# Optimization experiments

Hardware: AMD Instinct MI355X
Metric: run time of the kernel (lower is better)

Reference implementation:

```python
import jax, jax.numpy as jnp
import numpy as np

HIDDEN = 512
DETER = 1024
STOCH = 32
OBS = 1024
ACT = 64
B, T = 64, 256


def _linear_params(key, out_dim, in_dim):
    kw, kb = jax.random.split(key)
    scale = 1.0 / np.sqrt(in_dim)
    W = jax.random.uniform(kw, (out_dim, in_dim), jnp.float32, -scale, scale)
    b = jax.random.uniform(kb, (out_dim,), jnp.float32, -scale, scale)
    return W, b


def setup_inputs() -> dict:
    key = jax.random.key(0)
    ks = jax.random.split(key, 12)
    obs_embeds = jax.random.normal(ks[0], (B, T, OBS), jnp.float32)
    action_embs = jax.random.normal(ks[1], (B, T, ACT), jnp.float32)
    noise_prior = jax.random.normal(ks[2], (B, T, STOCH), jnp.float32)
    noise_post = jax.random.normal(ks[3], (B, T, STOCH), jnp.float32)
    W_sa, b_sa = _linear_params(ks[4], DETER, STOCH + ACT)
    W_ih, b_ih = _linear_params(ks[5], 3 * DETER, DETER)
    W_hh, b_hh = _linear_params(ks[6], 3 * DETER, DETER)
    Wp1, bp1 = _linear_params(ks[7], HIDDEN, DETER)
    Wp2, bp2 = _linear_params(ks[8], 2 * STOCH, HIDDEN)
    Wq1, bq1 = _linear_params(ks[9], HIDDEN, DETER + OBS)
    Wq2, bq2 = _linear_params(ks[10], 2 * STOCH, HIDDEN)
    return {
        "obs_embeds": obs_embeds, "action_embs": action_embs,
        "noise_prior": noise_prior, "noise_post": noise_post,
        "W_sa": W_sa, "b_sa": b_sa,
        "W_ih": W_ih, "b_ih": b_ih, "W_hh": W_hh, "b_hh": b_hh,
        "Wp1": Wp1, "bp1": bp1, "Wp2": Wp2, "bp2": bp2,
        "Wq1": Wq1, "bq1": bq1, "Wq2": Wq2, "bq2": bq2,
    }


def _rollout(obs_embeds, action_embs, noise_prior, noise_post,
             W_sa, b_sa, W_ih, b_ih, W_hh, b_hh,
             Wp1, bp1, Wp2, bp2, Wq1, bq1, Wq2, bq2):
    S = Wp2.shape[0] // 2
    eps = 1e-5

    def gru(x, h):  # torch GRUCell: gates ordered r, z, n
        gi = x @ W_ih.T + b_ih
        gh = h @ W_hh.T + b_hh
        ir, iz, inn = jnp.split(gi, 3, axis=-1)
        hr, hz, hn = jnp.split(gh, 3, axis=-1)
        r = jax.nn.sigmoid(ir + hr)
        z = jax.nn.sigmoid(iz + hz)
        n = jnp.tanh(inn + r * hn)
        return (1.0 - z) * n + z * h

    def step(carry, inp):
        deter, stoch = carry
        obs, act, n_p, n_q = inp
        # prior: h_t = f(s_{t-1}, a_{t-1}, h_{t-1})
        emb = jax.nn.relu(jnp.concatenate([stoch, act], -1) @ W_sa.T + b_sa)
        deter = gru(emb, deter)
        pm_s = jax.nn.relu(deter @ Wp1.T + bp1) @ Wp2.T + bp2
        p_mean = pm_s[..., :S]
        p_std = jax.nn.softplus(pm_s[..., S:]) + eps
        p_stoch = p_mean + p_std * n_p
        # posterior: p(s_t | h_t, o_t)
        qm_s = jax.nn.relu(jnp.concatenate([deter, obs], -1) @ Wq1.T + bq1) @ Wq2.T + bq2
        q_mean = qm_s[..., :S]
        q_std = jax.nn.softplus(qm_s[..., S:]) + eps
        q_stoch = q_mean + q_std * n_q
        out = jnp.concatenate([deter, p_mean, p_std, p_stoch, q_mean, q_std, q_stoch], -1)
        return (deter, q_stoch), out

    batch = obs_embeds.shape[0]
    deter0 = jnp.zeros((batch, W_hh.shape[1]), obs_embeds.dtype)
    stoch0 = jnp.zeros((batch, S), obs_embeds.dtype)
    xs = (
        jnp.swapaxes(obs_embeds, 0, 1),
        jnp.swapaxes(action_embs, 0, 1),
        jnp.swapaxes(noise_prior, 0, 1),
        jnp.swapaxes(noise_post, 0, 1),
    )
    _, outs = jax.lax.scan(step, (deter0, stoch0), xs)
    return jnp.swapaxes(outs, 0, 1)  # [B, T, deter + 6*stoch]


def reference(obs_embeds, action_embs, noise_prior, noise_post,
              W_sa, b_sa, W_ih, b_ih, W_hh, b_hh,
              Wp1, bp1, Wp2, bp2, Wq1, bq1, Wq2, bq2):
    return _rollout(obs_embeds, action_embs, noise_prior, noise_post,
                    W_sa, b_sa, W_ih, b_ih, W_hh, b_hh,
                    Wp1, bp1, Wp2, bp2, Wq1, bq1, Wq2, bq2)
```

## Files before the change

### kernel.cpp

```cpp
#include <hip/hip_runtime.h>
#include <math.h>

#define B_   64
#define T_   256
#define OUTD 1216
#define NBLK 64

typedef unsigned short ushort_t;
typedef unsigned int   uint32;
typedef unsigned long long u64;
typedef __attribute__((ext_vector_type(8))) short bfrag;
typedef __attribute__((ext_vector_type(4))) float f32x4;
typedef __attribute__((ext_vector_type(4))) unsigned short us4;

#define SCOPE_AGT __HIP_MEMORY_SCOPE_AGENT

__device__ __forceinline__ float sigmoidf_(float x) { return 1.0f / (1.0f + __expf(-x)); }
__device__ __forceinline__ float softplusf_(float x) { return (x > 20.0f) ? x : log1pf(__expf(x)); }
__device__ __forceinline__ ushort_t f2bf(float f) {
    uint32 u = __float_as_uint(f);
    u += 0x7fffu + ((u >> 16) & 1u);
    return (ushort_t)(u >> 16);
}
__device__ __forceinline__ float bf2f(ushort_t u) { return __uint_as_float(((uint32)u) << 16); }

union U16 { u64 q[2]; bfrag bv; f32x4 fv; };
union U8  { u64 q; us4 v4; };

__device__ __forceinline__ u64 ldc8(const void* p) {
    return __hip_atomic_load((const u64*)p, __ATOMIC_RELAXED, SCOPE_AGT);
}
__device__ __forceinline__ void stc8(void* p, u64 v) {
    __hip_atomic_store((u64*)p, v, __ATOMIC_RELAXED, SCOPE_AGT);
}
__device__ __forceinline__ f32x4 ldc16f(const void* p) {
    U16 u; u.q[0] = ldc8(p); u.q[1] = ldc8((const u64*)p + 1); return u.fv;
}
__device__ __forceinline__ void stc16f(void* p, f32x4 v) {
    U16 u; u.fv = v; stc8(p, u.q[0]); stc8((u64*)p + 1, u.q[1]);
}
__device__ __forceinline__ void stc16b(void* p, bfrag v) {
    U16 u; u.bv = v; stc8(p, u.q[0]); stc8((u64*)p + 1, u.q[1]);
}

__global__ void kwprep(const float* __restrict__ Wih, const float* __restrict__ Whh,
                       const float* __restrict__ Wp1, const float* __restrict__ Wq1,
                       const float* __restrict__ Wp2, const float* __restrict__ Wq2,
                       const float* __restrict__ Wsa,
                       ushort_t* Wih_b, ushort_t* Whh_b, ushort_t* Wp1_b, ushort_t* Wq1_b,
                       ushort_t* W2sw, ushort_t* Wsasw, unsigned* gsync) {
    int stride = gridDim.x * blockDim.x;
    int gid = blockIdx.x * blockDim.x + threadIdx.x;
    for (int i = gid; i < 4096; i += stride) gsync[i] = 0u;
    for (int i = gid; i < 3072 * 1024; i += stride) Wih_b[i] = f2bf(Wih[i]);
    for (int i = gid; i < 3072 * 1024; i += stride) Whh_b[i] = f2bf(Whh[i]);
    for (int i = gid; i < 512 * 1024; i += stride) Wp1_b[i] = f2bf(Wp1[i]);
    for (int i = gid; i < 512 * 2048; i += stride) Wq1_b[i] = f2bf(Wq1[i]);
    for (int i = gid; i < 65536; i += stride) {
        int head = i >> 15, g = (i >> 9) & 63, o = (i >> 3) & 63, ii = i & 7;
        const float* src = head ? Wq2 : Wp2;
        W2sw[i] = f2bf(src[o * 512 + g * 8 + ii]);
    }
    for (int i = gid; i < 98304; i += stride) {
        int g = i >> 13, j = (i >> 3) & 1023, ii = i & 7;
        Wsasw[i] = f2bf(Wsa[j * 96 + g * 8 + ii]);
    }
}

__device__ __forceinline__ void gbar(unsigned* gs, int blk, unsigned& ep) {
    asm volatile("s_waitcnt vmcnt(0)" ::: "memory");
    __syncthreads();
    ++ep;
    if (threadIdx.x == 0) {
        unsigned old = __hip_atomic_fetch_add(gs, 1u, __ATOMIC_RELAXED, SCOPE_AGT);
        if (old == ep * (unsigned)NBLK - 1u) {
#pragma unroll 8
            for (int i = 0; i < NBLK; ++i)
                __hip_atomic_store(gs + 64 + i * 32, ep, __ATOMIC_RELAXED, SCOPE_AGT);
        } else {
            unsigned* f = gs + 64 + blk * 32;
            while (__hip_atomic_load(f, __ATOMIC_RELAXED, SCOPE_AGT) < ep)
                __builtin_amdgcn_s_sleep(1);
        }
    }
    __syncthreads();
}

__global__ __launch_bounds__(512, 1) void krssm(
        const float* __restrict__ obs, const float* __restrict__ act,
        const float* __restrict__ n_p, const float* __restrict__ n_q,
        const float* __restrict__ Wsa, const float* __restrict__ bsa,
        const ushort_t* __restrict__ Wih, const ushort_t* __restrict__ Whh,
        const float* __restrict__ bih, const float* __restrict__ bhh,
        const ushort_t* __restrict__ Wp1b, const float* __restrict__ bp1,
        const ushort_t* __restrict__ Wq1b, const float* __restrict__ bq1,
        const ushort_t* __restrict__ W2sw, const ushort_t* __restrict__ Wsasw,
        const float* __restrict__ bp2, const float* __restrict__ bq2,
        ushort_t* emb_sw, ushort_t* obs_sw, ushort_t* det_sw,
        float* det_fp0, float* det_fp1,
        float* pm1, float* qm1, float* out, unsigned* gsync) {
    __shared__ float red[2 * 24 * 256];
    const int tid = threadIdx.x;
    const int blk = blockIdx.x;
    unsigned ep = 0;

    if (tid < 256) {
        const int b = blk;
        const int j0 = tid * 4;
        const float* arow_ = act + (size_t)b * T_ * 64;
        float accp[4];
#pragma unroll
        for (int jj = 0; jj < 4; ++jj) {
            int j = j0 + jj;
            float acc = bsa[j];
            const float* w = Wsa + j * 96 + 32;
#pragma unroll 8
            for (int c = 0; c < 64; ++c) acc += arow_[c] * w[c];
            accp[jj] = fmaxf(acc, 0.f);
        }
        U8 u;
#pragma unroll
        for (int jj = 0; jj < 4; ++jj) u.v4[jj] = f2bf(accp[jj]);
        size_t eoff = ((size_t)(j0 >> 3) * 64 + b) * 8 + (j0 & 7);
        stc8(emb_sw + eoff, u.q);
        stc8(det_sw + eoff, 0ull);
        *(f32x4*)(det_fp0 + blk * 1024 + tid * 4) = (f32x4){0.f, 0.f, 0.f, 0.f};
    } else if (tid < 384) {
        int g = tid - 256;
        const float* src = obs + (size_t)blk * T_ * 1024 + g * 8;
        bfrag v;
#pragma unroll
        for (int i = 0; i < 8; ++i) v[i] = (short)f2bf(src[i]);
        stc16b(obs_sw + ((size_t)g * 64 + blk) * 8, v);
    }
    gbar(gsync, blk, ep);

    float* dfp_in = det_fp0;
    float* dfp_out = det_fp1;

#pragma unroll 1
    for (int t = 0; t < T_; ++t) {
        const ushort_t* emb_t = emb_sw + ((size_t)t << 16);
        const ushort_t* det_t = det_sw + ((size_t)t << 16);
        ushort_t*       det_n = det_sw + ((size_t)(t + 1) << 16);
        const ushort_t* obs_t = obs_sw + ((size_t)t << 16);

        {
            const int lane = tid & 63, w = tid >> 6;
            const int kw = w >> 1, bw = w & 1;
            const int m = lane & 15, quad = lane >> 4;
            const int j0 = blk * 16;

            f32x4 acc[2][3][2];
#pragma unroll
            for (int a2 = 0; a2 < 2; ++a2)
#pragma unroll
                for (int g = 0; g < 3; ++g)
#pragma unroll
                    for (int n = 0; n < 2; ++n) acc[a2][g][n] = (f32x4){0.f, 0.f, 0.f, 0.f};

            const int kb0 = kw * 256;
            const ushort_t* arow[2][3];
#pragma unroll
            for (int g = 0; g < 3; ++g) {
                arow[0][g] = Wih + (size_t)(g * 1024 + j0 + m) * 1024 + kb0 + quad * 8;
                arow[1][g] = Whh + (size_t)(g * 1024 + j0 + m) * 1024 + kb0 + quad * 8;
            }
            const ushort_t* bx = emb_t + ((kb0 >> 3) + quad) * 512 + m * 8;
            const ushort_t* bh = det_t + ((kb0 >> 3) + quad) * 512 + m * 8;

#pragma unroll
            for (int it = 0; it < 8; ++it) {
                bfrag a[2][3], vx[2], vh[2];
#pragma unroll
                for (int g = 0; g < 3; ++g) {
                    a[0][g] = *(const bfrag*)(arow[0][g] + it * 32);
                    a[1][g] = *(const bfrag*)(arow[1][g] + it * 32);
                }
#pragma unroll
                for (int n = 0; n < 2; ++n) {
                    vx[n] = *(const bfrag*)(bx + it * 2048 + (bw * 2 + n) * 128);
                    vh[n] = *(const bfrag*)(bh + it * 2048 + (bw * 2 + n) * 128);
                }
#pragma unroll
                for (int g = 0; g < 3; ++g)
#pragma unroll
                    for (int n = 0; n < 2; ++n) {
                        acc[0][g][n] = __builtin_amdgcn_mfma_f32_16x16x32_bf16(a[0][g], vx[n], acc[0][g][n], 0, 0, 0);
                        acc[1][g][n] = __builtin_amdgcn_mfma_f32_16x16x32_bf16(a[1][g], vh[n], acc[1][g][n], 0, 0, 0);
                    }
            }

            if (kw & 1) {
                float* dst = red + (kw >> 1) * 6144;
#pragma unroll
                for (int a2 = 0; a2 < 2; ++a2)
#pragma unroll
                    for (int g = 0; g < 3; ++g)
#pragma unroll
                        for (int n = 0; n < 2; ++n)
                            *(f32x4*)(dst + ((a2 * 3 + g) * 4 + bw * 2 + n) * 256 + lane * 4) = acc[a2][g][n];
            }
            __syncthreads();
            if (!(kw & 1)) {
                float* dst = red + (kw >> 1) * 6144;
#pragma unroll
                for (int a2 = 0; a2 < 2; ++a2)
#pragma unroll
                    for (int g = 0; g < 3; ++g)
#pragma unroll
                        for (int n = 0; n < 2; ++n) {
                            float* pp = dst + ((a2 * 3 + g) * 4 + bw * 2 + n) * 256 + lane * 4;
                            f32x4 v = *(const f32x4*)pp;
                            v += acc[a2][g][n];
                            *(f32x4*)pp = v;
                        }
            }
            __syncthreads();

            if (tid < 256) {
                int b = tid >> 2, jq = tid & 3;
                int nt = b >> 4, bl = b & 15;
                int lsrc = (jq * 16 + bl) * 4;
                float gg[2][3][4];
#pragma unroll
                for (int a2 = 0; a2 < 2; ++a2)
#pragma unroll
                    for (int g = 0; g < 3; ++g) {
                        f32x4 v0 = *(const f32x4*)(red + ((a2 * 3 + g) * 4 + nt) * 256 + lsrc);
                        f32x4 v1 = *(const f32x4*)(red + 6144 + ((a2 * 3 + g) * 4 + nt) * 256 + lsrc);
#pragma unroll
                        for (int i = 0; i < 4; ++i) gg[a2][g][i] = v0[i] + v1[i];
                    }
                f32x4 bi[3], bh2[3];
#pragma unroll
                for (int g = 0; g < 3; ++g) {
                    bi[g] = *(const f32x4*)(bih + g * 1024 + j0 + jq * 4);
                    bh2[g] = *(const f32x4*)(bhh + g * 1024 + j0 + jq * 4);
                }
                f32x4 h4;
                U8 dq;
#pragma unroll
                for (int i = 0; i < 4; ++i) {
                    int j = j0 + jq * 4 + i;
                    float r = sigmoidf_(gg[0][0][i] + bi[0][i] + gg[1][0][i] + bh2[0][i]);
                    float z = sigmoidf_(gg[0][1][i] + bi[1][i] + gg[1][1][i] + bh2[1][i]);
                    float n = tanhf(gg[0][2][i] + bi[2][i] + r * (gg[1][2][i] + bh2[2][i]));
                    float hp = dfp_in[j * 64 + b];
                    float h = (1.f - z) * n + z * hp;
                    h4[i] = h;
                    dq.v4[i] = f2bf(h);
                    dfp_out[j * 64 + b] = h;
                }
                *(f32x4*)(out + ((size_t)b * T_ + t) * OUTD + j0 + jq * 4) = h4;
                int kbase = j0 + jq * 4;
                stc8(det_n + ((size_t)(kbase >> 3) * 64 + b) * 8 + (kbase & 7), dq.q);
            }
        }
        gbar(gsync, blk, ep);

        {
            const int lane = tid & 63, w = tid >> 6;
            const int kw = w >> 1, bw = w & 1;
            const int m = lane & 15, quad = lane >> 4;
            const bool isq = blk >= 32;
            const int j0 = (isq ? blk - 32 : blk) * 16;

            f32x4 acc[2];
            acc[0] = (f32x4){0.f, 0.f, 0.f, 0.f};
            acc[1] = (f32x4){0.f, 0.f, 0.f, 0.f};

            if (!isq) {
                const ushort_t* ar = Wp1b + (size_t)(j0 + m) * 1024 + kw * 256 + quad * 8;
                const ushort_t* bb = det_n + ((kw * 32) + quad) * 512 + m * 8;
#pragma unroll
                for (int it = 0; it < 8; ++it) {
                    bfrag a = *(const bfrag*)(ar + it * 32);
#pragma unroll
                    for (int n = 0; n < 2; ++n) {
                        bfrag v = *(const bfrag*)(bb + it * 2048 + (bw * 2 + n) * 128);
                        acc[n] = __builtin_amdgcn_mfma_f32_16x16x32_bf16(a, v, acc[n], 0, 0, 0);
                    }
                }
            } else {
                int kb0 = kw * 512;
                const ushort_t* bsrc = (kw < 2) ? (const ushort_t*)det_n : obs_t;
                int kloc = (kw < 2) ? kb0 : kb0 - 1024;
                const ushort_t* ar = Wq1b + (size_t)(j0 + m) * 2048 + kb0 + quad * 8;
                const ushort_t* bb = bsrc + ((kloc >> 3) + quad) * 512 + m * 8;
#pragma unroll
                for (int it = 0; it < 16; ++it) {
                    bfrag a = *(const bfrag*)(ar + it * 32);
#pragma unroll
                    for (int n = 0; n < 2; ++n) {
                        bfrag v = *(const bfrag*)(bb + it * 2048 + (bw * 2 + n) * 128);
                        acc[n] = __builtin_amdgcn_mfma_f32_16x16x32_bf16(a, v, acc[n], 0, 0, 0);
                    }
                }
            }
#pragma unroll
            for (int n = 0; n < 2; ++n)
                *(f32x4*)(red + (kw * 4 + bw * 2 + n) * 256 + lane * 4) = acc[n];
            __syncthreads();

            if (tid < 256) {
                int b = tid >> 2, jq = tid & 3;
                int nt = b >> 4, lsrc = (jq * 16 + (b & 15)) * 4;
                f32x4 s = (f32x4){0.f, 0.f, 0.f, 0.f};
#pragma unroll
                for (int w2 = 0; w2 < 4; ++w2) s += *(const f32x4*)(red + (w2 * 4 + nt) * 256 + lsrc);
                f32x4 bv = *(const f32x4*)((isq ? bq1 : bp1) + j0 + jq * 4);
                f32x4 r;
#pragma unroll
                for (int i = 0; i < 4; ++i) r[i] = fmaxf(s[i] + bv[i], 0.f);
                stc16f((isq ? qm1 : pm1) + (size_t)b * 512 + j0 + jq * 4, r);
            }
        }
        gbar(gsync, blk, ep);

        {
            float* s_p = red;
            float* s_q = red + 512;
            float* s_in = red + 1152;
            float* ph = red + 1280;
            ushort_t* ush = (ushort_t*)(red + 1536);
            const int b = blk;
            if (tid < 128) ((f32x4*)s_p)[tid] = ldc16f(pm1 + (size_t)b * 512 + tid * 4);
            else if (tid < 256) ((f32x4*)s_q)[tid - 128] = ldc16f(qm1 + (size_t)b * 512 + (tid - 128) * 4);
            else if (tid < 384) {
                if (t + 1 < T_) {
                    int g = tid - 256;
                    const float* src0 = obs + ((size_t)b * T_ + t + 1) * 1024 + g * 8;
                    bfrag v0;
#pragma unroll
                    for (int i = 0; i < 8; ++i) v0[i] = (short)f2bf(src0[i]);
                    stc16b(obs_sw + ((size_t)(t + 1) << 16) + ((size_t)g * 64 + b) * 8, v0);
                }
            } else if (tid < 448) {
                if (t + 1 < T_) s_in[32 + (tid - 384)] = act[((size_t)b * T_ + t + 1) * 64 + (tid - 384)];
            }
            __syncthreads();
            if (tid < 256) {
                int kh = tid >> 7, head = (tid >> 6) & 1, o = tid & 63;
                const ushort_t* wp = W2sw + head * 32768 + o * 8 + kh * 32 * 512;
                const float* hv = (head ? s_q : s_p) + kh * 256;
                float acc2 = 0.f;
#pragma unroll 8
                for (int g = 0; g < 32; ++g) {
                    bfrag w8 = *(const bfrag*)(wp + g * 512);
#pragma unroll
                    for (int i2 = 0; i2 < 8; ++i2) acc2 += hv[g * 8 + i2] * bf2f((ushort_t)w8[i2]);
                }
                ph[kh * 128 + head * 64 + o] = acc2;
            }
            __syncthreads();
            if (tid < 64) {
                int s = tid & 31, isq = tid >> 5;
                const float* bias = isq ? bq2 : bp2;
                float mean = ph[isq * 64 + s] + ph[128 + isq * 64 + s] + bias[s];
                float raw  = ph[isq * 64 + 32 + s] + ph[128 + isq * 64 + 32 + s] + bias[32 + s];
                float sd = softplusf_(raw) + 1e-5f;
                float noise = (isq ? n_q : n_p)[((size_t)b * T_ + t) * 32 + s];
                float st = mean + sd * noise;
                float* o = out + ((size_t)b * T_ + t) * OUTD + 1024 + isq * 96;
                o[s] = mean;
                o[32 + s] = sd;
                o[64 + s] = st;
                if (isq) s_in[s] = st;
            }
            __syncthreads();
            if (t + 1 < T_) {
                int j0e = tid * 2;
                float acc2[2];
                acc2[0] = bsa[j0e];
                acc2[1] = bsa[j0e + 1];
#pragma unroll
                for (int g = 0; g < 12; ++g) {
#pragma unroll
                    for (int jj = 0; jj < 2; ++jj) {
                        bfrag w8 = *(const bfrag*)(Wsasw + ((size_t)g * 1024 + j0e + jj) * 8);
#pragma unroll
                        for (int i2 = 0; i2 < 8; ++i2) acc2[jj] += s_in[g * 8 + i2] * bf2f((ushort_t)w8[i2]);
                    }
                }
                ush[j0e] = f2bf(fmaxf(acc2[0], 0.f));
                ush[j0e + 1] = f2bf(fmaxf(acc2[1], 0.f));
            }
            __syncthreads();
            if (t + 1 < T_ && tid < 128) {
                bfrag v = *(const bfrag*)(ush + tid * 8);
                stc16b(emb_sw + ((size_t)(t + 1) << 16) + ((size_t)tid * 64 + b) * 8, v);
            }
        }
        gbar(gsync, blk, ep);

        float* tf = dfp_in; dfp_in = dfp_out; dfp_out = tf;
    }
}

extern "C" void kernel_launch(void* const* d_in, const int* in_sizes, int n_in,
                              void* d_out, int out_size, void* d_ws, size_t ws_size,
                              hipStream_t stream) {
    const float* obs = (const float*)d_in[0];
    const float* act = (const float*)d_in[1];
    const float* n_p = (const float*)d_in[2];
    const float* n_q = (const float*)d_in[3];
    const float* W_sa = (const float*)d_in[4];
    const float* b_sa = (const float*)d_in[5];
    const float* W_ih = (const float*)d_in[6];
    const float* b_ih = (const float*)d_in[7];
    const float* W_hh = (const float*)d_in[8];
    const float* b_hh = (const float*)d_in[9];
    const float* Wp1 = (const float*)d_in[10];
    const float* bp1 = (const float*)d_in[11];
    const float* Wp2 = (const float*)d_in[12];
    const float* bp2 = (const float*)d_in[13];
    const float* Wq1 = (const float*)d_in[14];
    const float* bq1 = (const float*)d_in[15];
    const float* Wq2 = (const float*)d_in[16];
    const float* bq2 = (const float*)d_in[17];
    float* out = (float*)d_out;

    if (ws_size < (size_t)115 * 1024 * 1024) return;

    char* p = (char*)d_ws;
    ushort_t* Wih_b = (ushort_t*)p;  p += (size_t)3145728 * 2;
    ushort_t* Whh_b = (ushort_t*)p;  p += (size_t)3145728 * 2;
    ushort_t* Wp1_b = (ushort_t*)p;  p += (size_t)524288 * 2;
    ushort_t* Wq1_b = (ushort_t*)p;  p += (size_t)1048576 * 2;
    ushort_t* W2sw  = (ushort_t*)p;  p += (size_t)65536 * 2;
    ushort_t* Wsasw = (ushort_t*)p;  p += (size_t)98304 * 2;
    float* pm1 = (float*)p; p += (size_t)32768 * 4;
    float* qm1 = (float*)p; p += (size_t)32768 * 4;
    float* det_fp0 = (float*)p; p += (size_t)65536 * 4;
    float* det_fp1 = (float*)p; p += (size_t)65536 * 4;
    unsigned* gsync = (unsigned*)p; p += (size_t)16384 * 4;
    ushort_t* emb_sw = (ushort_t*)p; p += (size_t)256 * 65536 * 2;
    ushort_t* obs_sw = (ushort_t*)p; p += (size_t)256 * 65536 * 2;
    ushort_t* det_sw = (ushort_t*)p; p += (size_t)257 * 65536 * 2;

    kwprep<<<1024, 256, 0, stream>>>(W_ih, W_hh, Wp1, Wq1, Wp2, Wq2, W_sa,
                                     Wih_b, Whh_b, Wp1_b, Wq1_b, W2sw, Wsasw, gsync);
    krssm<<<NBLK, 512, 0, stream>>>(obs, act, n_p, n_q, W_sa, b_sa,
                                    Wih_b, Whh_b, b_ih, b_hh,
                                    Wp1_b, bp1, Wq1_b, bq1,
                                    W2sw, Wsasw, bp2, bq2,
                                    emb_sw, obs_sw, det_sw,
                                    det_fp0, det_fp1, pm1, qm1, out, gsync);
}
```

Before: 11.82 ms.

## Compute prior/posterior hidden layers per batch block and replace counter barrier with flag barrier

The p1/q1 hidden layers were split across blocks by output column, which needed a global barrier and a round trip through global memory. Now each block computes the full 512-wide hidden layers for its own batch row from det/obs staged in shared memory. That removes one grid barrier per timestep and the pm1/qm1 buffers. The grid barrier also changes from an atomic counter with a broadcast to per-block epoch flags that 64 lanes poll. The cost is that every block now streams all of Wp1 and Wq1 per step (about 3MB bf16) using only one useful MFMA column, so redundant weight traffic and wasted MFMA work rise sharply.

Result: slower. 39.05 ms (+230.3%).

```diff
diff --git a/kernel.cpp b/kernel.cpp
--- a/kernel.cpp
+++ b/kernel.cpp
@@ -27,17 +27,8 @@
 union U16 { u64 q[2]; bfrag bv; f32x4 fv; };
 union U8  { u64 q; us4 v4; };
 
-__device__ __forceinline__ u64 ldc8(const void* p) {
-    return __hip_atomic_load((const u64*)p, __ATOMIC_RELAXED, SCOPE_AGT);
-}
 __device__ __forceinline__ void stc8(void* p, u64 v) {
     __hip_atomic_store((u64*)p, v, __ATOMIC_RELAXED, SCOPE_AGT);
-}
-__device__ __forceinline__ f32x4 ldc16f(const void* p) {
-    U16 u; u.q[0] = ldc8(p); u.q[1] = ldc8((const u64*)p + 1); return u.fv;
-}
-__device__ __forceinline__ void stc16f(void* p, f32x4 v) {
-    U16 u; u.fv = v; stc8(p, u.q[0]); stc8((u64*)p + 1, u.q[1]);
 }
 __device__ __forceinline__ void stc16b(void* p, bfrag v) {
     U16 u; u.bv = v; stc8(p, u.q[0]); stc8((u64*)p + 1, u.q[1]);
@@ -71,17 +62,12 @@
     asm volatile("s_waitcnt vmcnt(0)" ::: "memory");
     __syncthreads();
     ++ep;
-    if (threadIdx.x == 0) {
-        unsigned old = __hip_atomic_fetch_add(gs, 1u, __ATOMIC_RELAXED, SCOPE_AGT);
-        if (old == ep * (unsigned)NBLK - 1u) {
-#pragma unroll 8
-            for (int i = 0; i < NBLK; ++i)
-                __hip_atomic_store(gs + 64 + i * 32, ep, __ATOMIC_RELAXED, SCOPE_AGT);
-        } else {
-            unsigned* f = gs + 64 + blk * 32;
-            while (__hip_atomic_load(f, __ATOMIC_RELAXED, SCOPE_AGT) < ep)
-                __builtin_amdgcn_s_sleep(1);
-        }
+    if (threadIdx.x < 64) {
+        if (threadIdx.x == 0)
+            __hip_atomic_store(gs + 64 + blk * 32, ep, __ATOMIC_RELAXED, SCOPE_AGT);
+        while (__hip_atomic_load(gs + 64 + (int)threadIdx.x * 32,
+                                 __ATOMIC_RELAXED, SCOPE_AGT) < ep)
+            __builtin_amdgcn_s_sleep(1);
     }
     __syncthreads();
 }
@@ -98,7 +84,7 @@
         const float* __restrict__ bp2, const float* __restrict__ bq2,
         ushort_t* emb_sw, ushort_t* obs_sw, ushort_t* det_sw,
         float* det_fp0, float* det_fp1,
-        float* pm1, float* qm1, float* out, unsigned* gsync) {
+        float* out, unsigned* gsync) {
     __shared__ float red[2 * 24 * 256];
     const int tid = threadIdx.x;
     const int blk = blockIdx.x;
@@ -260,74 +246,23 @@
         gbar(gsync, blk, ep);
 
         {
-            const int lane = tid & 63, w = tid >> 6;
-            const int kw = w >> 1, bw = w & 1;
-            const int m = lane & 15, quad = lane >> 4;
-            const bool isq = blk >= 32;
-            const int j0 = (isq ? blk - 32 : blk) * 16;
-
-            f32x4 acc[2];
-            acc[0] = (f32x4){0.f, 0.f, 0.f, 0.f};
-            acc[1] = (f32x4){0.f, 0.f, 0.f, 0.f};
-
-            if (!isq) {
-                const ushort_t* ar = Wp1b + (size_t)(j0 + m) * 1024 + kw * 256 + quad * 8;
-                const ushort_t* bb = det_n + ((kw * 32) + quad) * 512 + m * 8;
-#pragma unroll
-                for (int it = 0; it < 8; ++it) {
-                    bfrag a = *(const bfrag*)(ar + it * 32);
-#pragma unroll
-                    for (int n = 0; n < 2; ++n) {
-                        bfrag v = *(const bfrag*)(bb + it * 2048 + (bw * 2 + n) * 128);
-                        acc[n] = __builtin_amdgcn_mfma_f32_16x16x32_bf16(a, v, acc[n], 0, 0, 0);
-                    }
-                }
-            } else {
-                int kb0 = kw * 512;
-                const ushort_t* bsrc = (kw < 2) ? (const ushort_t*)det_n : obs_t;
-                int kloc = (kw < 2) ? kb0 : kb0 - 1024;
-                const ushort_t* ar = Wq1b + (size_t)(j0 + m) * 2048 + kb0 + quad * 8;
-                const ushort_t* bb = bsrc + ((kloc >> 3) + quad) * 512 + m * 8;
-#pragma unroll
-                for (int it = 0; it < 16; ++it) {
-                    bfrag a = *(const bfrag*)(ar + it * 32);
-#pragma unroll
-                    for (int n = 0; n < 2; ++n) {
-                        bfrag v = *(const bfrag*)(bb + it * 2048 + (bw * 2 + n) * 128);
-                        acc[n] = __builtin_amdgcn_mfma_f32_16x16x32_bf16(a, v, acc[n], 0, 0, 0);
-                    }
-                }
-            }
-#pragma unroll
-            for (int n = 0; n < 2; ++n)
-                *(f32x4*)(red + (kw * 4 + bw * 2 + n) * 256 + lane * 4) = acc[n];
-            __syncthreads();
-
-            if (tid < 256) {
-                int b = tid >> 2, jq = tid & 3;
-                int nt = b >> 4, lsrc = (jq * 16 + (b & 15)) * 4;
-                f32x4 s = (f32x4){0.f, 0.f, 0.f, 0.f};
-#pragma unroll
-                for (int w2 = 0; w2 < 4; ++w2) s += *(const f32x4*)(red + (w2 * 4 + nt) * 256 + lsrc);
-                f32x4 bv = *(const f32x4*)((isq ? bq1 : bp1) + j0 + jq * 4);
-                f32x4 r;
-#pragma unroll
-                for (int i = 0; i < 4; ++i) r[i] = fmaxf(s[i] + bv[i], 0.f);
-                stc16f((isq ? qm1 : pm1) + (size_t)b * 512 + j0 + jq * 4, r);
-            }
-        }
-        gbar(gsync, blk, ep);
-
-        {
-            float* s_p = red;
-            float* s_q = red + 512;
-            float* s_in = red + 1152;
-            float* ph = red + 1280;
-            ushort_t* ush = (ushort_t*)(red + 1536);
+            ushort_t* s_det = (ushort_t*)red;
+            ushort_t* s_obs = (ushort_t*)(red + 512);
+            float* s_pm = red + 1024;
+            float* s_qm = red + 1536;
+            float* ph   = red + 2048;
+            float* s_in = red + 2304;
+            ushort_t* ush = (ushort_t*)(red + 2432);
             const int b = blk;
-            if (tid < 128) ((f32x4*)s_p)[tid] = ldc16f(pm1 + (size_t)b * 512 + tid * 4);
-            else if (tid < 256) ((f32x4*)s_q)[tid - 128] = ldc16f(qm1 + (size_t)b * 512 + (tid - 128) * 4);
-            else if (tid < 384) {
+
+            if (tid < 128) {
+                bfrag v = *(const bfrag*)(det_n + ((size_t)tid * 64 + b) * 8);
+                *(bfrag*)(s_det + tid * 8) = v;
+            } else if (tid < 256) {
+                int g = tid - 128;
+                bfrag v = *(const bfrag*)(obs_t + ((size_t)g * 64 + b) * 8);
+                *(bfrag*)(s_obs + g * 8) = v;
+            } else if (tid < 384) {
                 if (t + 1 < T_) {
                     int g = tid - 256;
                     const float* src0 = obs + ((size_t)b * T_ + t + 1) * 1024 + g * 8;
@@ -340,10 +275,55 @@
                 if (t + 1 < T_) s_in[32 + (tid - 384)] = act[((size_t)b * T_ + t + 1) * 64 + (tid - 384)];
             }
             __syncthreads();
+
+            {
+                const int lane = tid & 63, w = tid >> 6;
+                const int m = lane & 15, quad = lane >> 4;
+#pragma unroll
+                for (int rep = 0; rep < 4; ++rep) {
+                    int j0 = (w + rep * 8) * 16;
+                    f32x4 acc = (f32x4){0.f, 0.f, 0.f, 0.f};
+                    const ushort_t* ar = Wp1b + (size_t)(j0 + m) * 1024 + quad * 8;
+#pragma unroll
+                    for (int kb = 0; kb < 32; ++kb) {
+                        bfrag a = *(const bfrag*)(ar + kb * 32);
+                        bfrag bv = *(const bfrag*)(s_det + kb * 32 + quad * 8);
+                        acc = __builtin_amdgcn_mfma_f32_16x16x32_bf16(a, bv, acc, 0, 0, 0);
+                    }
+                    if (m == 0) {
+                        int jr = j0 + quad * 4;
+#pragma unroll
+                        for (int i = 0; i < 4; ++i)
+                            s_pm[jr + i] = fmaxf(acc[i] + bp1[jr + i], 0.f);
+                    }
+                }
+#pragma unroll
+                for (int rep = 0; rep < 4; ++rep) {
+                    int j0 = (w + rep * 8) * 16;
+                    f32x4 acc = (f32x4){0.f, 0.f, 0.f, 0.f};
+                    const ushort_t* ar = Wq1b + (size_t)(j0 + m) * 2048 + quad * 8;
+#pragma unroll
+                    for (int kb = 0; kb < 64; ++kb) {
+                        bfrag a = *(const bfrag*)(ar + kb * 32);
+                        const ushort_t* bs = (kb < 32) ? (s_det + kb * 32)
+                                                       : (s_obs + (kb - 32) * 32);
+                        bfrag bv = *(const bfrag*)(bs + quad * 8);
+                        acc = __builtin_amdgcn_mfma_f32_16x16x32_bf16(a, bv, acc, 0, 0, 0);
+                    }
+                    if (m == 0) {
+                        int jr = j0 + quad * 4;
+#pragma unroll
+                        for (int i = 0; i < 4; ++i)
+                            s_qm[jr + i] = fmaxf(acc[i] + bq1[jr + i], 0.f);
+                    }
+                }
+            }
+            __syncthreads();
+
             if (tid < 256) {
                 int kh = tid >> 7, head = (tid >> 6) & 1, o = tid & 63;
                 const ushort_t* wp = W2sw + head * 32768 + o * 8 + kh * 32 * 512;
-                const float* hv = (head ? s_q : s_p) + kh * 256;
+                const float* hv = (head ? s_qm : s_pm) + kh * 256;
                 float acc2 = 0.f;
 #pragma unroll 8
                 for (int g = 0; g < 32; ++g) {
@@ -421,7 +401,7 @@
     const float* bq2 = (const float*)d_in[17];
     float* out = (float*)d_out;
 
-    if (ws_size < (size_t)115 * 1024 * 1024) return;
+    if (ws_size < (size_t)114 * 1024 * 1024) return;
 
     char* p = (char*)d_ws;
     ushort_t* Wih_b = (ushort_t*)p;  p += (size_t)3145728 * 2;
@@ -430,8 +410,6 @@
     ushort_t* Wq1_b = (ushort_t*)p;  p += (size_t)1048576 * 2;
     ushort_t* W2sw  = (ushort_t*)p;  p += (size_t)65536 * 2;
     ushort_t* Wsasw = (ushort_t*)p;  p += (size_t)98304 * 2;
-    float* pm1 = (float*)p; p += (size_t)32768 * 4;
-    float* qm1 = (float*)p; p += (size_t)32768 * 4;
     float* det_fp0 = (float*)p; p += (size_t)65536 * 4;
     float* det_fp1 = (float*)p; p += (size_t)65536 * 4;
     unsigned* gsync = (unsigned*)p; p += (size_t)16384 * 4;
@@ -446,5 +424,5 @@
                                     Wp1_b, bp1, Wq1_b, bq1,
                                     W2sw, Wsasw, bp2, bq2,
                                     emb_sw, obs_sw, det_sw,
-                                    det_fp0, det_fp1, pm1, qm1, out, gsync);
-}
+                                    det_fp0, det_fp1, out, gsync);
+}
```
